# Kernel optimization log

Hardware: AMD Instinct MI355X
Metric: run time of the kernel (lower is better)

The kernel has to match this reference:

```python
import jax, jax.numpy as jnp
import numpy as np

D = 65
CHUNK = 64
K = 64
SCALE = D ** (-0.5)

def gelu(x):
    return jax.nn.gelu(x, approximate=False)  # torch nn.GELU default is exact erf

def setup_inputs() -> dict:
    key = jax.random.key(0)
    ks = jax.random.split(key, 16)
    B, N = 32, 16384
    s = SCALE
    return {
        "x": jax.random.normal(ks[0], (B, N, D), jnp.float32),
        # query_gen: Linear(D,D) -> GELU -> Linear(D, K*D)
        "Wq1": jax.random.normal(ks[1], (D, D), jnp.float32) * s,
        "bq1": jnp.zeros((D,), jnp.float32),
        "Wq2": jax.random.normal(ks[2], (D, K * D), jnp.float32) * s,
        "bq2": jnp.zeros((K * D,), jnp.float32),
        "Wk": jax.random.normal(ks[3], (D, D), jnp.float32) * s,
        "bk": jnp.zeros((D,), jnp.float32),
        "Wv": jax.random.normal(ks[4], (D, D), jnp.float32) * s,
        "bv": jnp.zeros((D,), jnp.float32),
        "cross_q": jax.random.normal(ks[5], (1, D), jnp.float32) * s,
        "pos_enc": jax.random.normal(ks[6], (1, CHUNK, D), jnp.float32) * s,
        "Wr": jax.random.normal(ks[7], (D, D), jnp.float32) * (1.0 / np.sqrt(D)),
        "br": jnp.zeros((D,), jnp.float32),
        "gamma": jnp.ones((D,), jnp.float32),
        "beta": jnp.zeros((D,), jnp.float32),
    }

def reference(x, Wq1, bq1, Wq2, bq2, Wk, bk, Wv, bv, cross_q, pos_enc, Wr, br, gamma, beta):
    B, N, d = x.shape
    nb = N // CHUNK  # N chosen divisible by CHUNK -> mask is all True, pad branch skipped

    # global average (mask all-ones => plain mean over N)
    gavg = jnp.mean(x, axis=1)  # [B, D]

    # queries: MLP on global average, reshape to [B, K, D], scaled
    q = (gelu(gavg @ Wq1 + bq1) @ Wq2 + bq2).reshape(B, K, d) * SCALE

    # keys / values: Linear + GELU, chunked, + positional encoding per chunk
    keys = gelu(x @ Wk + bk).reshape(B, nb, CHUNK, d) + pos_enc[None]      # [B,nb,C,D]
    values = gelu(x @ Wv + bv).reshape(B, nb, CHUNK, d) + pos_enc[None]    # [B,nb,C,D]

    # block-local attention (mask is all-True, masked_fill is a no-op)
    scores = jnp.einsum('bkd,bncd->bnkc', q, keys) * SCALE                 # [B,nb,K,C]
    w = jax.nn.softmax(scores, axis=-1)                                    # dropout = eval-mode identity
    blk = jnp.einsum('bnkc,bncd->bnkd', w, values)                         # [B,nb,K,D]
    blk = jnp.transpose(blk, (0, 2, 1, 3))                                 # [B,K,nb,D]

    # cross-block attention with a single learned query
    cs = jnp.einsum('d,bknd->bkn', cross_q[0], blk) * SCALE                # [B,K,nb]
    cw = jax.nn.softmax(cs, axis=-1)
    compressed = jnp.einsum('bkn,bknd->bkd', cw, blk)                      # [B,K,D]

    # residual + LayerNorm
    compressed = compressed + (gavg @ Wr + br)[:, None, :]
    mu = jnp.mean(compressed, axis=-1, keepdims=True)
    var = jnp.var(compressed, axis=-1, keepdims=True)
    return (compressed - mu) * jax.lax.rsqrt(var + 1e-5) * gamma + beta
```

## Files before the change

kernel.cpp:

```cpp
#include <hip/hip_runtime.h>
#include <hip/hip_bf16.h>

#define BATCH 32
#define NSEQ  16384
#define DDIM  65
#define CHUNK 64
#define KQ    64
#define NBLK  256
#define SCALE 0.12403473458920847f

typedef __bf16 bf16x8 __attribute__((ext_vector_type(8)));
typedef float  f32x4  __attribute__((ext_vector_type(4)));
#define MFMA16(a, b, c) __builtin_amdgcn_mfma_f32_16x16x32_bf16(a, b, c, 0, 0, 0)

#define BLK_ROWSTRIDE 72
#define BLK_CHUNKSTRIDE (64 * 72)
#define BLK_BSTRIDE ((size_t)NBLK * 64 * 72)

__device__ __forceinline__ float gelu_exact(float v) {
    return 0.5f * v * (1.0f + erff(v * 0.7071067811865476f));
}

__device__ __forceinline__ float gelu_tanh(float x) {
    float x2 = x * x;
    float t  = 0.7978845608028654f * x * fmaf(0.044715f, x2, 1.0f);
    float e  = __expf(2.0f * t);
    float th = 1.0f - 2.0f * __builtin_amdgcn_rcpf(e + 1.0f);
    return 0.5f * x * (1.0f + th);
}

__global__ __launch_bounds__(320) void k_gavg(const float* __restrict__ x,
                                              float* __restrict__ partial,
                                              const float* __restrict__ Wk,
                                              const float* __restrict__ Wv,
                                              __bf16* __restrict__ WkT,
                                              __bf16* __restrict__ WvT) {
    const int tid = threadIdx.x;
    if (blockIdx.y == 32) {
        const int i = blockIdx.x * 320 + tid;
        const int m = i / 5120;
        const int j = i - m * 5120;
        const int d = j >> 6, e = j & 63;
        const float* W = m ? Wv : Wk;
        __bf16* T = m ? WvT : WkT;
        T[(size_t)d * 64 + e] = (d < DDIM) ? (__bf16)W[e * DDIM + d]
                                           : (__bf16)0.0f;
        return;
    }
    const int s = blockIdx.x;
    const int b = blockIdx.y;
    const int g = tid / 65;
    const int j = tid - g * 65;
    const bool active = tid < 260;
    float acc[4] = {0.f, 0.f, 0.f, 0.f};
    if (active) {
        const float4* p = (const float4*)(x + (size_t)b * NSEQ * DDIM
                                            + (size_t)s * 512 * DDIM);
        #pragma unroll 8
        for (int it = 0; it < 32; ++it) {
            const float4 v = p[(it * 4 + g) * 65 + j];
            acc[0] += v.x; acc[1] += v.y; acc[2] += v.z; acc[3] += v.w;
        }
    }
    __shared__ float lds[4][65][4];
    if (active) {
        lds[g][j][0] = acc[0]; lds[g][j][1] = acc[1];
        lds[g][j][2] = acc[2]; lds[g][j][3] = acc[3];
    }
    __syncthreads();
    if (tid < DDIM) {
        float a = 0.f;
        #pragma unroll
        for (int rr = 0; rr < 4; ++rr) {
            const int f = tid + 65 * rr;
            const int jj = f >> 2, ee = f & 3;
            a += lds[0][jj][ee] + lds[1][jj][ee]
               + lds[2][jj][ee] + lds[3][jj][ee];
        }
        partial[((size_t)b * 32 + s) * DDIM + tid] = a;
    }
}

__global__ __launch_bounds__(256) void k_qgen1(const float* __restrict__ partial,
    const float* __restrict__ Wq1, const float* __restrict__ bq1,
    const float* __restrict__ Wr,  const float* __restrict__ br,
    float* __restrict__ h_out, float* __restrict__ r_out) {
    const int b = blockIdx.x, tid = threadIdx.x;
    __shared__ float g[DDIM];
    if (tid < DDIM) {
        float a = 0.f;
        const float* p = partial + (size_t)b * 32 * DDIM + tid;
        #pragma unroll 8
        for (int s = 0; s < 32; ++s) a += p[s * DDIM];
        g[tid] = a * (1.0f / 16384.0f);
    }
    __syncthreads();
    if (tid < DDIM) {
        float a = bq1[tid];
        for (int e = 0; e < DDIM; ++e) a += g[e] * Wq1[e * DDIM + tid];
        h_out[b * DDIM + tid] = gelu_exact(a);
    } else if (tid >= 128 && tid < 128 + DDIM) {
        const int d = tid - 128;
        float a = br[d];
        for (int e = 0; e < DDIM; ++e) a += g[e] * Wr[e * DDIM + d];
        r_out[b * DDIM + d] = a;
    }
}

__global__ __launch_bounds__(256) void k_qgen2(const float* __restrict__ h_in,
    const float* __restrict__ Wq2, const float* __restrict__ bq2,
    __bf16* __restrict__ qbf, float* __restrict__ q64) {
    const int b = blockIdx.y, tid = threadIdx.x;
    const int o = blockIdx.x * 256 + tid;
    __shared__ float h[DDIM];
    if (tid < DDIM) h[tid] = h_in[b * DDIM + tid];
    __syncthreads();
    if (o >= KQ * DDIM) return;
    float a = bq2[o];
    #pragma unroll 13
    for (int e = 0; e < DDIM; ++e) a += h[e] * Wq2[e * (KQ * DDIM) + o];
    a *= SCALE;
    const int k = o / DDIM, d = o - k * DDIM;
    if (d < 64) qbf[(size_t)b * 4096 + k * 64 + d] = (__bf16)a;
    else        q64[b * 64 + k] = a;
}

__global__ __launch_bounds__(256, 5) void k_attn(const float* __restrict__ x,
    const __bf16* __restrict__ qbf, const float* __restrict__ q64,
    const __bf16* __restrict__ WkT, const __bf16* __restrict__ WvT,
    const float* __restrict__ Wk, const float* __restrict__ bkb,
    const float* __restrict__ Wv, const float* __restrict__ bvb,
    const float* __restrict__ pos, const float* __restrict__ cq,
    __bf16* __restrict__ blk_out, float* __restrict__ cs_out) {
    const int nb = blockIdx.x;
    const int b  = blockIdx.y;
    const int tid = threadIdx.x;
    const int lane = tid & 63, w = tid >> 6;
    const int l16 = lane & 15, quad = lane >> 4;

    __shared__ __align__(16) __bf16 xsP[64 * 72];
    __shared__ __align__(16) __bf16 keys[64 * 72];
    __shared__ __align__(16) __bf16 valsT[64 * 72];
    __shared__ float vals64[64];
    __shared__ float xs64[64];

    __bf16* blk_row = blk_out + (size_t)b * BLK_BSTRIDE
                              + (size_t)nb * BLK_CHUNKSTRIDE;

    {
        const int c = tid >> 2, g = tid & 3;
        const float* xrow = x + ((size_t)b * NSEQ + (size_t)nb * CHUNK + c) * DDIM;
        __bf16* dst = xsP + c * 72;
        #pragma unroll
        for (int j = 0; j < 16; ++j)
            dst[g + 4 * j] = (__bf16)xrow[g + 4 * j];
        if (g == 0) xs64[c] = xrow[64];
    }
    __syncthreads();

    {
        const __bf16* arow = xsP + (w * 16 + l16) * 72 + quad * 8;
        bf16x8 a0 = *(const bf16x8*)arow;
        bf16x8 a1 = *(const bf16x8*)(arow + 32);
        f32x4 ak[5], av[5];
        const f32x4 z = {0.f, 0.f, 0.f, 0.f};
        #pragma unroll
        for (int nt = 0; nt < 5; ++nt) {
            const __bf16* bkr = WkT + (nt * 16 + l16) * 64 + quad * 8;
            const __bf16* bvr = WvT + (nt * 16 + l16) * 64 + quad * 8;
            ak[nt] = MFMA16(a0, *(const bf16x8*)bkr, z);
            ak[nt] = MFMA16(a1, *(const bf16x8*)(bkr + 32), ak[nt]);
            av[nt] = MFMA16(a0, *(const bf16x8*)bvr, z);
            av[nt] = MFMA16(a1, *(const bf16x8*)(bvr + 32), av[nt]);
        }
        float xe[4];
        #pragma unroll
        for (int r = 0; r < 4; ++r) xe[r] = xs64[w * 16 + quad * 4 + r];
        #pragma unroll
        for (int nt = 0; nt < 5; ++nt) {
            const int d = nt * 16 + l16;
            if (d <= 64) {
                const float wk64d = Wk[64 * DDIM + d];
                const float wv64d = Wv[64 * DDIM + d];
                const float bkd = bkb[d], bvd = bvb[d];
                #pragma unroll
                for (int r = 0; r < 4; ++r) {
                    const int c = w * 16 + quad * 4 + r;
                    const float pv = pos[c * DDIM + d];
                    const float kvv = gelu_tanh(ak[nt][r] + xe[r] * wk64d + bkd) + pv;
                    const float vvv = gelu_tanh(av[nt][r] + xe[r] * wv64d + bvd) + pv;
                    keys[c * 72 + d] = (__bf16)kvv;
                    if (d < 64) valsT[d * 72 + c] = (__bf16)vvv;
                    else        vals64[c] = vvv;
                }
            }
        }
    }
    __syncthreads();

    float csr[4];
    {
        const __bf16* aq = qbf + (size_t)b * 4096 + (w * 16 + l16) * 64 + quad * 8;
        bf16x8 qa0 = *(const bf16x8*)aq;
        bf16x8 qa1 = *(const bf16x8*)(aq + 32);
        const f32x4 z = {0.f, 0.f, 0.f, 0.f};
        float q64k[4];
        #pragma unroll
        for (int r = 0; r < 4; ++r) q64k[r] = q64[b * 64 + w * 16 + quad * 4 + r];
        float st[4][4];
        #pragma unroll
        for (int nt = 0; nt < 4; ++nt) {
            const __bf16* kb = keys + (nt * 16 + l16) * 72 + quad * 8;
            f32x4 sacc = MFMA16(qa0, *(const bf16x8*)kb, z);
            sacc = MFMA16(qa1, *(const bf16x8*)(kb + 32), sacc);
            const float k64c = (float)keys[(nt * 16 + l16) * 72 + 64];
            #pragma unroll
            for (int r = 0; r < 4; ++r)
                st[nt][r] = fmaf(q64k[r], k64c, sacc[r]) * SCALE;
        }
        float mr[4], sum[4], inv[4];
        #pragma unroll
        for (int r = 0; r < 4; ++r) {
            float m = fmaxf(fmaxf(st[0][r], st[1][r]), fmaxf(st[2][r], st[3][r]));
            m = fmaxf(m, __shfl_xor(m, 1));
            m = fmaxf(m, __shfl_xor(m, 2));
            m = fmaxf(m, __shfl_xor(m, 4));
            m = fmaxf(m, __shfl_xor(m, 8));
            mr[r] = m;
            sum[r] = 0.f;
        }
        #pragma unroll
        for (int nt = 0; nt < 4; ++nt)
            #pragma unroll
            for (int r = 0; r < 4; ++r) {
                st[nt][r] = __expf(st[nt][r] - mr[r]);
                sum[r] += st[nt][r];
            }
        #pragma unroll
        for (int r = 0; r < 4; ++r) {
            float s = sum[r];
            s += __shfl_xor(s, 1);
            s += __shfl_xor(s, 2);
            s += __shfl_xor(s, 4);
            s += __shfl_xor(s, 8);
            inv[r] = __builtin_amdgcn_rcpf(s);
        }
        #pragma unroll
        for (int nt = 0; nt < 4; ++nt)
            #pragma unroll
            for (int r = 0; r < 4; ++r)
                xsP[(w * 16 + quad * 4 + r) * 72 + nt * 16 + l16] =
                    (__bf16)(st[nt][r] * inv[r]);
        float v64l[4];
        #pragma unroll
        for (int nt = 0; nt < 4; ++nt) v64l[nt] = vals64[nt * 16 + l16];
        const float cq64 = cq[64];
        #pragma unroll
        for (int r = 0; r < 4; ++r) {
            float o = st[0][r] * v64l[0];
            o = fmaf(st[1][r], v64l[1], o);
            o = fmaf(st[2][r], v64l[2], o);
            o = fmaf(st[3][r], v64l[3], o);
            o += __shfl_xor(o, 1);
            o += __shfl_xor(o, 2);
            o += __shfl_xor(o, 4);
            o += __shfl_xor(o, 8);
            csr[r] = 0.f;
            if (l16 == 0) {
                const float o64 = o * inv[r];
                const int k = w * 16 + quad * 4 + r;
                bf16x8 v8;
                #pragma unroll
                for (int i2 = 0; i2 < 8; ++i2) v8[i2] = (__bf16)0.0f;
                v8[0] = (__bf16)o64;
                *(bf16x8*)(blk_row + k * BLK_ROWSTRIDE + 64) = v8;
                csr[r] = o64 * cq64;
            }
        }
    }
    __syncthreads();

    {
        const __bf16* pr = xsP + (w * 16 + l16) * 72 + quad * 8;
        bf16x8 pa0 = *(const bf16x8*)pr;
        bf16x8 pa1 = *(const bf16x8*)(pr + 32);
        const f32x4 z = {0.f, 0.f, 0.f, 0.f};
        #pragma unroll
        for (int nt = 0; nt < 4; ++nt) {
            const __bf16* vb = valsT + (nt * 16 + l16) * 72 + quad * 8;
            f32x4 o = MFMA16(pa0, *(const bf16x8*)vb, z);
            o = MFMA16(pa1, *(const bf16x8*)(vb + 32), o);
            const int d = nt * 16 + l16;
            const float cqd = cq[d];
            #pragma unroll
            for (int r = 0; r < 4; ++r) {
                const int k = w * 16 + quad * 4 + r;
                blk_row[k * BLK_ROWSTRIDE + d] = (__bf16)o[r];
                csr[r] = fmaf(o[r], cqd, csr[r]);
            }
        }
        #pragma unroll
        for (int r = 0; r < 4; ++r) {
            float v = csr[r];
            v += __shfl_xor(v, 1);
            v += __shfl_xor(v, 2);
            v += __shfl_xor(v, 4);
            v += __shfl_xor(v, 8);
            if (l16 == 0) {
                const int k = w * 16 + quad * 4 + r;
                cs_out[((size_t)b * KQ + k) * NBLK + nb] = v * SCALE;
            }
        }
    }
}

__global__ __launch_bounds__(256) void k_cross(
    const __bf16* __restrict__ blk, const float* __restrict__ cs,
    const float* __restrict__ rres, const float* __restrict__ gamma,
    const float* __restrict__ beta, float* __restrict__ out) {
    const int bk_ = blockIdx.x;
    const int b = bk_ >> 6, k = bk_ & 63;
    const int tid = threadIdx.x;
    const int w = tid >> 6, lane = tid & 63;

    __shared__ float ew[NBLK];
    __shared__ float wredA[4];
    __shared__ float lred[252][8];
    __shared__ float vv[DDIM];
    __shared__ float stats[2];

    const float v = cs[(size_t)bk_ * NBLK + tid];
    float m = v;
    for (int off = 32; off; off >>= 1) m = fmaxf(m, __shfl_down(m, off));
    if (lane == 0) wredA[w] = m;
    __syncthreads();
    m = fmaxf(fmaxf(wredA[0], wredA[1]), fmaxf(wredA[2], wredA[3]));
    const float e = __expf(v - m);
    ew[tid] = e;
    float s = e;
    for (int off = 32; off; off >>= 1) s += __shfl_down(s, off);
    __syncthreads();
    if (lane == 0) wredA[w] = s;
    __syncthreads();
    const float inv = 1.0f / (wredA[0] + wredA[1] + wredA[2] + wredA[3]);

    const int g = tid / 9, seg = tid - g * 9;
    float acc[8] = {0.f, 0.f, 0.f, 0.f, 0.f, 0.f, 0.f, 0.f};
    if (tid < 252) {
        const __bf16* base = blk + (size_t)b * BLK_BSTRIDE
                                 + k * BLK_ROWSTRIDE + seg * 8;
        #pragma unroll 2
        for (int it = 0; it < 10; ++it) {
            const int r = it * 28 + g;
            if (r < NBLK) {
                bf16x8 vx = *(const bf16x8*)(base + (size_t)r * BLK_CHUNKSTRIDE);
                const float wg = ew[r];
                #pragma unroll
                for (int i2 = 0; i2 < 8; ++i2)
                    acc[i2] = fmaf(wg, (float)vx[i2], acc[i2]);
            }
        }
        #pragma unroll
        for (int i2 = 0; i2 < 8; ++i2) lred[tid][i2] = acc[i2];
    }
    __syncthreads();
    if (tid < 72) {
        const int sg = tid >> 3, i2 = tid & 7;
        float a = 0.f;
        #pragma unroll 7
        for (int gg = 0; gg < 28; ++gg) a += lred[gg * 9 + sg][i2];
        const int d = sg * 8 + i2;
        if (d < DDIM) vv[d] = a * inv + rres[b * DDIM + d];
    }
    __syncthreads();
    if (tid < 64) {
        float a  = vv[tid] + (tid == 0 ? vv[64] : 0.f);
        float sq = vv[tid] * vv[tid] + (tid == 0 ? vv[64] * vv[64] : 0.f);
        for (int off = 32; off; off >>= 1) {
            a  += __shfl_down(a, off);
            sq += __shfl_down(sq, off);
        }
        if (tid == 0) {
            const float mu  = a * (1.0f / DDIM);
            const float var = sq * (1.0f / DDIM) - mu * mu;
            stats[0] = mu;
            stats[1] = rsqrtf(var + 1e-5f);
        }
    }
    __syncthreads();
    if (tid < DDIM) {
        out[(size_t)bk_ * DDIM + tid] =
            (vv[tid] - stats[0]) * stats[1] * gamma[tid] + beta[tid];
    }
}

extern "C" void kernel_launch(void* const* d_in, const int* in_sizes, int n_in,
                              void* d_out, int out_size, void* d_ws, size_t ws_size,
                              hipStream_t stream) {
    const float* x    = (const float*)d_in[0];
    const float* Wq1  = (const float*)d_in[1];
    const float* bq1  = (const float*)d_in[2];
    const float* Wq2  = (const float*)d_in[3];
    const float* bq2  = (const float*)d_in[4];
    const float* Wk   = (const float*)d_in[5];
    const float* bk   = (const float*)d_in[6];
    const float* Wv   = (const float*)d_in[7];
    const float* bv   = (const float*)d_in[8];
    const float* cq   = (const float*)d_in[9];
    const float* pos  = (const float*)d_in[10];
    const float* Wr   = (const float*)d_in[11];
    const float* br   = (const float*)d_in[12];
    const float* gamma= (const float*)d_in[13];
    const float* beta = (const float*)d_in[14];
    float* out = (float*)d_out;

    char* w8 = (char*)d_ws;
    __bf16* blk     = (__bf16*)w8;
    float*  partial = (float*)w8;
    float*  rres    = (float*)(w8 + 75497472);
    float*  q64     = (float*)(w8 + 75505792);
    float*  hbuf    = (float*)(w8 + 75513984);
    float*  cs      = (float*)(w8 + 75522304);
    __bf16* qbf     = (__bf16*)(w8 + 77619456);
    __bf16* WkT     = (__bf16*)(w8 + 77881600);
    __bf16* WvT     = (__bf16*)(w8 + 77891840);

    k_gavg<<<dim3(32, 33), 320, 0, stream>>>(x, partial, Wk, Wv, WkT, WvT);
    k_qgen1<<<BATCH, 256, 0, stream>>>(partial, Wq1, bq1, Wr, br, hbuf, rres);
    k_qgen2<<<dim3(17, BATCH), 256, 0, stream>>>(hbuf, Wq2, bq2, qbf, q64);
    k_attn<<<dim3(NBLK, BATCH), 256, 0, stream>>>(x, qbf, q64, WkT, WvT,
                                                  Wk, bk, Wv, bv, pos, cq,
                                                  blk, cs);
    k_cross<<<BATCH * KQ, 256, 0, stream>>>(blk, cs, rres, gamma, beta, out);
}
```

Before: 378.0 us.

## Fuse query-generation kernels and alias LDS buffers in attention kernel

Merges the two query-generation kernels into one per-batch kernel that keeps the hidden vector in shared memory, removing a launch and a global round-trip. The attention kernel drops its separate x/probability staging buffer and reuses the keys buffer instead, which adds a barrier after the scores are computed. This shrinks shared memory so the launch bound can be raised from 5 to 8 blocks per CU. The fused qgen now runs on only 32 blocks, so the second matvec has far less parallelism than the old 17x32 grid.

```diff
diff --git a/kernel.cpp b/kernel.cpp
--- a/kernel.cpp
+++ b/kernel.cpp
@@ -81,12 +81,14 @@
     }
 }
 
-__global__ __launch_bounds__(256) void k_qgen1(const float* __restrict__ partial,
+__global__ __launch_bounds__(256) void k_qgen(const float* __restrict__ partial,
     const float* __restrict__ Wq1, const float* __restrict__ bq1,
+    const float* __restrict__ Wq2, const float* __restrict__ bq2,
     const float* __restrict__ Wr,  const float* __restrict__ br,
-    float* __restrict__ h_out, float* __restrict__ r_out) {
+    __bf16* __restrict__ qbf, float* __restrict__ q64,
+    float* __restrict__ r_out) {
     const int b = blockIdx.x, tid = threadIdx.x;
-    __shared__ float g[DDIM];
+    __shared__ float g[DDIM], h[DDIM];
     if (tid < DDIM) {
         float a = 0.f;
         const float* p = partial + (size_t)b * 32 * DDIM + tid;
@@ -98,34 +100,26 @@
     if (tid < DDIM) {
         float a = bq1[tid];
         for (int e = 0; e < DDIM; ++e) a += g[e] * Wq1[e * DDIM + tid];
-        h_out[b * DDIM + tid] = gelu_exact(a);
+        h[tid] = gelu_exact(a);
     } else if (tid >= 128 && tid < 128 + DDIM) {
         const int d = tid - 128;
         float a = br[d];
         for (int e = 0; e < DDIM; ++e) a += g[e] * Wr[e * DDIM + d];
         r_out[b * DDIM + d] = a;
     }
-}
-
-__global__ __launch_bounds__(256) void k_qgen2(const float* __restrict__ h_in,
-    const float* __restrict__ Wq2, const float* __restrict__ bq2,
-    __bf16* __restrict__ qbf, float* __restrict__ q64) {
-    const int b = blockIdx.y, tid = threadIdx.x;
-    const int o = blockIdx.x * 256 + tid;
-    __shared__ float h[DDIM];
-    if (tid < DDIM) h[tid] = h_in[b * DDIM + tid];
-    __syncthreads();
-    if (o >= KQ * DDIM) return;
-    float a = bq2[o];
-    #pragma unroll 13
-    for (int e = 0; e < DDIM; ++e) a += h[e] * Wq2[e * (KQ * DDIM) + o];
-    a *= SCALE;
-    const int k = o / DDIM, d = o - k * DDIM;
-    if (d < 64) qbf[(size_t)b * 4096 + k * 64 + d] = (__bf16)a;
-    else        q64[b * 64 + k] = a;
-}
-
-__global__ __launch_bounds__(256, 5) void k_attn(const float* __restrict__ x,
+    __syncthreads();
+    for (int o = tid; o < KQ * DDIM; o += 256) {
+        float a = bq2[o];
+        #pragma unroll 13
+        for (int e = 0; e < DDIM; ++e) a += h[e] * Wq2[e * (KQ * DDIM) + o];
+        a *= SCALE;
+        const int k = o / DDIM, d = o - k * DDIM;
+        if (d < 64) qbf[(size_t)b * 4096 + k * 64 + d] = (__bf16)a;
+        else        q64[b * 64 + k] = a;
+    }
+}
+
+__global__ __launch_bounds__(256, 8) void k_attn(const float* __restrict__ x,
     const __bf16* __restrict__ qbf, const float* __restrict__ q64,
     const __bf16* __restrict__ WkT, const __bf16* __restrict__ WvT,
     const float* __restrict__ Wk, const float* __restrict__ bkb,
@@ -138,7 +132,6 @@
     const int lane = tid & 63, w = tid >> 6;
     const int l16 = lane & 15, quad = lane >> 4;
 
-    __shared__ __align__(16) __bf16 xsP[64 * 72];
     __shared__ __align__(16) __bf16 keys[64 * 72];
     __shared__ __align__(16) __bf16 valsT[64 * 72];
     __shared__ float vals64[64];
@@ -150,7 +143,7 @@
     {
         const int c = tid >> 2, g = tid & 3;
         const float* xrow = x + ((size_t)b * NSEQ + (size_t)nb * CHUNK + c) * DDIM;
-        __bf16* dst = xsP + c * 72;
+        __bf16* dst = keys + c * 72;
         #pragma unroll
         for (int j = 0; j < 16; ++j)
             dst[g + 4 * j] = (__bf16)xrow[g + 4 * j];
@@ -159,7 +152,7 @@
     __syncthreads();
 
     {
-        const __bf16* arow = xsP + (w * 16 + l16) * 72 + quad * 8;
+        const __bf16* arow = keys + (w * 16 + l16) * 72 + quad * 8;
         bf16x8 a0 = *(const bf16x8*)arow;
         bf16x8 a1 = *(const bf16x8*)(arow + 32);
         f32x4 ak[5], av[5];
@@ -173,9 +166,8 @@
             av[nt] = MFMA16(a0, *(const bf16x8*)bvr, z);
             av[nt] = MFMA16(a1, *(const bf16x8*)(bvr + 32), av[nt]);
         }
-        float xe[4];
-        #pragma unroll
-        for (int r = 0; r < 4; ++r) xe[r] = xs64[w * 16 + quad * 4 + r];
+        const float4 xe4 = *(const float4*)(xs64 + w * 16 + quad * 4);
+        const float xe[4] = {xe4.x, xe4.y, xe4.z, xe4.w};
         #pragma unroll
         for (int nt = 0; nt < 5; ++nt) {
             const int d = nt * 16 + l16;
@@ -198,16 +190,15 @@
     }
     __syncthreads();
 
-    float csr[4];
+    float st[4][4];
+    float inv[4];
     {
         const __bf16* aq = qbf + (size_t)b * 4096 + (w * 16 + l16) * 64 + quad * 8;
         bf16x8 qa0 = *(const bf16x8*)aq;
         bf16x8 qa1 = *(const bf16x8*)(aq + 32);
         const f32x4 z = {0.f, 0.f, 0.f, 0.f};
-        float q64k[4];
-        #pragma unroll
-        for (int r = 0; r < 4; ++r) q64k[r] = q64[b * 64 + w * 16 + quad * 4 + r];
-        float st[4][4];
+        const float4 q4 = *(const float4*)(q64 + b * 64 + w * 16 + quad * 4);
+        const float q64k[4] = {q4.x, q4.y, q4.z, q4.w};
         #pragma unroll
         for (int nt = 0; nt < 4; ++nt) {
             const __bf16* kb = keys + (nt * 16 + l16) * 72 + quad * 8;
@@ -218,7 +209,7 @@
             for (int r = 0; r < 4; ++r)
                 st[nt][r] = fmaf(q64k[r], k64c, sacc[r]) * SCALE;
         }
-        float mr[4], sum[4], inv[4];
+        float mr[4], sum[4];
         #pragma unroll
         for (int r = 0; r < 4; ++r) {
             float m = fmaxf(fmaxf(st[0][r], st[1][r]), fmaxf(st[2][r], st[3][r]));
@@ -245,11 +236,16 @@
             s += __shfl_xor(s, 8);
             inv[r] = __builtin_amdgcn_rcpf(s);
         }
+    }
+    __syncthreads();
+
+    float csr[4];
+    {
         #pragma unroll
         for (int nt = 0; nt < 4; ++nt)
             #pragma unroll
             for (int r = 0; r < 4; ++r)
-                xsP[(w * 16 + quad * 4 + r) * 72 + nt * 16 + l16] =
+                keys[(w * 16 + quad * 4 + r) * 72 + nt * 16 + l16] =
                     (__bf16)(st[nt][r] * inv[r]);
         float v64l[4];
         #pragma unroll
@@ -278,10 +274,9 @@
             }
         }
     }
-    __syncthreads();
 
     {
-        const __bf16* pr = xsP + (w * 16 + l16) * 72 + quad * 8;
+        const __bf16* pr = keys + (w * 16 + l16) * 72 + quad * 8;
         bf16x8 pa0 = *(const bf16x8*)pr;
         bf16x8 pa1 = *(const bf16x8*)(pr + 32);
         const f32x4 z = {0.f, 0.f, 0.f, 0.f};
@@ -419,15 +414,14 @@
     float*  partial = (float*)w8;
     float*  rres    = (float*)(w8 + 75497472);
     float*  q64     = (float*)(w8 + 75505792);
-    float*  hbuf    = (float*)(w8 + 75513984);
-    float*  cs      = (float*)(w8 + 75522304);
-    __bf16* qbf     = (__bf16*)(w8 + 77619456);
-    __bf16* WkT     = (__bf16*)(w8 + 77881600);
-    __bf16* WvT     = (__bf16*)(w8 + 77891840);
+    float*  cs      = (float*)(w8 + 75513984);
+    __bf16* qbf     = (__bf16*)(w8 + 77611136);
+    __bf16* WkT     = (__bf16*)(w8 + 77873280);
+    __bf16* WvT     = (__bf16*)(w8 + 77883520);
 
     k_gavg<<<dim3(32, 33), 320, 0, stream>>>(x, partial, Wk, Wv, WkT, WvT);
-    k_qgen1<<<BATCH, 256, 0, stream>>>(partial, Wq1, bq1, Wr, br, hbuf, rres);
-    k_qgen2<<<dim3(17, BATCH), 256, 0, stream>>>(hbuf, Wq2, bq2, qbf, q64);
+    k_qgen<<<BATCH, 256, 0, stream>>>(partial, Wq1, bq1, Wq2, bq2, Wr, br,
+                                      qbf, q64, rres);
     k_attn<<<dim3(NBLK, BATCH), 256, 0, stream>>>(x, qbf, q64, WkT, WvT,
                                                   Wk, bk, Wv, bv, pos, cq,
                                                   blk, cs);
```

New measurement: 430.4 us. 1.14x slower.

## Alias x and P buffers onto keys LDS and hoist per-column constant loads

Applied to the files above, without the earlier changes.

Drops the separate xsP shared buffer and reuses the keys tile for the staged x chunk and later for the softmax probabilities. An extra barrier is added between score computation and the P write so keys are not overwritten while other waves still read them. Per-column Wk/Wv row-64, bias and positional-encoding values are loaded into registers before the x staging. Scalar loads of xs64 and q64 become float4 loads, and the min-blocks launch bound is removed. The aim is lower LDS use per block for higher occupancy and hidden global-load latency, at the cost of more live registers and one more barrier.

```diff
diff --git a/kernel.cpp b/kernel.cpp
--- a/kernel.cpp
+++ b/kernel.cpp
@@ -125,7 +125,7 @@
     else        q64[b * 64 + k] = a;
 }
 
-__global__ __launch_bounds__(256, 5) void k_attn(const float* __restrict__ x,
+__global__ __launch_bounds__(256) void k_attn(const float* __restrict__ x,
     const __bf16* __restrict__ qbf, const float* __restrict__ q64,
     const __bf16* __restrict__ WkT, const __bf16* __restrict__ WvT,
     const float* __restrict__ Wk, const float* __restrict__ bkb,
@@ -138,7 +138,6 @@
     const int lane = tid & 63, w = tid >> 6;
     const int l16 = lane & 15, quad = lane >> 4;
 
-    __shared__ __align__(16) __bf16 xsP[64 * 72];
     __shared__ __align__(16) __bf16 keys[64 * 72];
     __shared__ __align__(16) __bf16 valsT[64 * 72];
     __shared__ float vals64[64];
@@ -147,10 +146,26 @@
     __bf16* blk_row = blk_out + (size_t)b * BLK_BSTRIDE
                               + (size_t)nb * BLK_CHUNKSTRIDE;
 
+    float wk64v[5], wv64v[5], bkv[5], bvv[5], posv[5][4];
+    {
+        #pragma unroll
+        for (int nt = 0; nt < 5; ++nt) {
+            const int d = nt * 16 + l16;
+            const int dc = d > 64 ? 64 : d;
+            wk64v[nt] = Wk[64 * DDIM + dc];
+            wv64v[nt] = Wv[64 * DDIM + dc];
+            bkv[nt]   = bkb[dc];
+            bvv[nt]   = bvb[dc];
+            #pragma unroll
+            for (int r = 0; r < 4; ++r)
+                posv[nt][r] = pos[(w * 16 + quad * 4 + r) * DDIM + dc];
+        }
+    }
+
     {
         const int c = tid >> 2, g = tid & 3;
         const float* xrow = x + ((size_t)b * NSEQ + (size_t)nb * CHUNK + c) * DDIM;
-        __bf16* dst = xsP + c * 72;
+        __bf16* dst = keys + c * 72;
         #pragma unroll
         for (int j = 0; j < 16; ++j)
             dst[g + 4 * j] = (__bf16)xrow[g + 4 * j];
@@ -159,7 +174,7 @@
     __syncthreads();
 
     {
-        const __bf16* arow = xsP + (w * 16 + l16) * 72 + quad * 8;
+        const __bf16* arow = keys + (w * 16 + l16) * 72 + quad * 8;
         bf16x8 a0 = *(const bf16x8*)arow;
         bf16x8 a1 = *(const bf16x8*)(arow + 32);
         f32x4 ak[5], av[5];
@@ -173,22 +188,18 @@
             av[nt] = MFMA16(a0, *(const bf16x8*)bvr, z);
             av[nt] = MFMA16(a1, *(const bf16x8*)(bvr + 32), av[nt]);
         }
-        float xe[4];
-        #pragma unroll
-        for (int r = 0; r < 4; ++r) xe[r] = xs64[w * 16 + quad * 4 + r];
+        const float4 xe4 = *(const float4*)(xs64 + w * 16 + quad * 4);
+        const float xe[4] = {xe4.x, xe4.y, xe4.z, xe4.w};
         #pragma unroll
         for (int nt = 0; nt < 5; ++nt) {
             const int d = nt * 16 + l16;
             if (d <= 64) {
-                const float wk64d = Wk[64 * DDIM + d];
-                const float wv64d = Wv[64 * DDIM + d];
-                const float bkd = bkb[d], bvd = bvb[d];
                 #pragma unroll
                 for (int r = 0; r < 4; ++r) {
                     const int c = w * 16 + quad * 4 + r;
-                    const float pv = pos[c * DDIM + d];
-                    const float kvv = gelu_tanh(ak[nt][r] + xe[r] * wk64d + bkd) + pv;
-                    const float vvv = gelu_tanh(av[nt][r] + xe[r] * wv64d + bvd) + pv;
+                    const float pv = posv[nt][r];
+                    const float kvv = gelu_tanh(fmaf(xe[r], wk64v[nt], ak[nt][r]) + bkv[nt]) + pv;
+                    const float vvv = gelu_tanh(fmaf(xe[r], wv64v[nt], av[nt][r]) + bvv[nt]) + pv;
                     keys[c * 72 + d] = (__bf16)kvv;
                     if (d < 64) valsT[d * 72 + c] = (__bf16)vvv;
                     else        vals64[c] = vvv;
@@ -198,16 +209,15 @@
     }
     __syncthreads();
 
-    float csr[4];
+    float st[4][4];
+    float inv[4];
     {
         const __bf16* aq = qbf + (size_t)b * 4096 + (w * 16 + l16) * 64 + quad * 8;
         bf16x8 qa0 = *(const bf16x8*)aq;
         bf16x8 qa1 = *(const bf16x8*)(aq + 32);
         const f32x4 z = {0.f, 0.f, 0.f, 0.f};
-        float q64k[4];
-        #pragma unroll
-        for (int r = 0; r < 4; ++r) q64k[r] = q64[b * 64 + w * 16 + quad * 4 + r];
-        float st[4][4];
+        const float4 q4 = *(const float4*)(q64 + b * 64 + w * 16 + quad * 4);
+        const float q64k[4] = {q4.x, q4.y, q4.z, q4.w};
         #pragma unroll
         for (int nt = 0; nt < 4; ++nt) {
             const __bf16* kb = keys + (nt * 16 + l16) * 72 + quad * 8;
@@ -218,7 +228,7 @@
             for (int r = 0; r < 4; ++r)
                 st[nt][r] = fmaf(q64k[r], k64c, sacc[r]) * SCALE;
         }
-        float mr[4], sum[4], inv[4];
+        float mr[4], sum[4];
         #pragma unroll
         for (int r = 0; r < 4; ++r) {
             float m = fmaxf(fmaxf(st[0][r], st[1][r]), fmaxf(st[2][r], st[3][r]));
@@ -245,11 +255,16 @@
             s += __shfl_xor(s, 8);
             inv[r] = __builtin_amdgcn_rcpf(s);
         }
+    }
+    __syncthreads();
+
+    float csr[4];
+    {
         #pragma unroll
         for (int nt = 0; nt < 4; ++nt)
             #pragma unroll
             for (int r = 0; r < 4; ++r)
-                xsP[(w * 16 + quad * 4 + r) * 72 + nt * 16 + l16] =
+                keys[(w * 16 + quad * 4 + r) * 72 + nt * 16 + l16] =
                     (__bf16)(st[nt][r] * inv[r]);
         float v64l[4];
         #pragma unroll
@@ -278,10 +293,9 @@
             }
         }
     }
-    __syncthreads();
-
-    {
-        const __bf16* pr = xsP + (w * 16 + l16) * 72 + quad * 8;
+
+    {
+        const __bf16* pr = keys + (w * 16 + l16) * 72 + quad * 8;
         bf16x8 pa0 = *(const bf16x8*)pr;
         bf16x8 pa1 = *(const bf16x8*)(pr + 32);
         const f32x4 z = {0.f, 0.f, 0.f, 0.f};
```

Result: no change. 380.9 us (+0.8%).
